# Optimization experiments

Measured on AMD Instinct MI355X. Metric: run time of the kernel, lower is better.

The kernel has to match this reference:

```python
import jax, jax.numpy as jnp
import numpy as np

FP8_MAX = 448.0  # finfo(float8_e4m3fn).max

def setup_inputs() -> dict:
    key = jax.random.key(0)
    k_x, k_w, k_b = jax.random.split(key, 3)
    B, S, D_IN, D_OUT = 4, 2048, 4096, 16384
    x = jax.random.normal(k_x, (B, S, D_IN), dtype=jnp.float32)
    # Build an fp8-quantized weight exactly as FP8WeightOnlyLinear.from_linear does:
    w = jax.random.normal(k_w, (D_OUT, D_IN), dtype=jnp.float32) * 0.02
    amax = jnp.max(jnp.abs(w))
    scale = jnp.where(amax > 0, amax / FP8_MAX, 1.0)
    # round-trip through float8_e4m3fn so stored values are true fp8 codes
    w_fp8 = jnp.clip(w / scale, -FP8_MAX, FP8_MAX).astype(jnp.float8_e4m3fn)
    weight_fp8 = w_fp8.astype(jnp.float32)  # fp8-representable values, held in fp32
    weight_scale = scale.reshape(1).astype(jnp.float32)
    bias = jax.random.normal(k_b, (D_OUT,), dtype=jnp.float32) * 0.01
    return {"x": x, "weight_fp8": weight_fp8, "weight_scale": weight_scale, "bias": bias}

def reference(x, weight_fp8, weight_scale, bias):
    # w = weight_fp8.to(x.dtype) * weight_scale ; out = x @ w.T + bias
    w = weight_fp8.astype(x.dtype) * weight_scale.astype(x.dtype)  # [D_OUT, D_IN]
    out = jnp.einsum('bsd,od->bso', x, w) + bias.astype(x.dtype)
    return out
```

## Files before the change

kernel.cpp:

```cpp
#include <hip/hip_runtime.h>
#include <stdint.h>

typedef unsigned int u32;
using i32x4 = __attribute__((ext_vector_type(4))) int;

#define GLD_LDS16(SRC, DST)                                      \
  __builtin_amdgcn_global_load_lds(                              \
      (const __attribute__((address_space(1))) void*)(SRC),      \
      (__attribute__((address_space(3))) void*)(DST), 16, 0, 0)

#define SCHED0() __builtin_amdgcn_sched_barrier(0)
#define BAR()    __builtin_amdgcn_s_barrier()
#define PRIO(x)  __builtin_amdgcn_s_setprio(x)

__global__ __launch_bounds__(256)
void quant_rows(const float* __restrict__ x, const float* __restrict__ w,
                signed char* __restrict__ xq, signed char* __restrict__ wq,
                float* __restrict__ sx, float* __restrict__ sw,
                int Mrows, int totRows, int K) {
  __shared__ float red[4];
  for (int row = blockIdx.x; row < totRows; row += gridDim.x) {
    const bool isx = row < Mrows;
    const float* src = isx ? x + (size_t)row * K : w + (size_t)(row - Mrows) * K;
    const float4* s4 = reinterpret_cast<const float4*>(src) + threadIdx.x * 4;
    float4 v[4];
#pragma unroll
    for (int g = 0; g < 4; ++g) v[g] = s4[g];
    float am = 0.f;
#pragma unroll
    for (int g = 0; g < 4; ++g)
      am = fmaxf(am, fmaxf(fmaxf(fabsf(v[g].x), fabsf(v[g].y)),
                           fmaxf(fabsf(v[g].z), fabsf(v[g].w))));
#pragma unroll
    for (int m = 1; m <= 32; m <<= 1) am = fmaxf(am, __shfl_xor(am, m));
    if ((threadIdx.x & 63) == 0) red[threadIdx.x >> 6] = am;
    __syncthreads();
    am = fmaxf(fmaxf(red[0], red[1]), fmaxf(red[2], red[3]));
    const float s   = am > 0.f ? am * (1.f / 127.f) : 1.f;
    const float inv = am > 0.f ? 127.f / am : 0.f;
    u32 pk[4];
#pragma unroll
    for (int g = 0; g < 4; ++g) {
      const float* vp = reinterpret_cast<const float*>(&v[g]);
      u32 p = 0;
#pragma unroll
      for (int e = 0; e < 4; ++e) {
        int q = (int)rintf(vp[e] * inv);
        q = q < -127 ? -127 : (q > 127 ? 127 : q);
        p |= ((u32)(q & 0xff)) << (8 * e);
      }
      pk[g] = p;
    }
    signed char* dst = (isx ? xq + (size_t)row * K : wq + (size_t)(row - Mrows) * K)
                       + threadIdx.x * 16;
    *reinterpret_cast<uint4*>(dst) = make_uint4(pk[0], pk[1], pk[2], pk[3]);
    if (threadIdx.x == 0) { if (isx) sx[row] = s; else sw[row - Mrows] = s; }
    __syncthreads();
  }
}

__global__ __launch_bounds__(512, 2)
void gemm_i8(const signed char* __restrict__ A,
             const signed char* __restrict__ B,
             const float* __restrict__ sx,
             const float* __restrict__ sw,
             const float* __restrict__ wscale_p,
             const float* __restrict__ bias,
             float* __restrict__ C,
             int Nn, int Kk, int NT) {
  __shared__ signed char lds[2][2][256 * 64];

  const int tid  = threadIdx.x;
  const int lane = tid & 63;
  const int wave = tid >> 6;
  const int wr = wave >> 2;
  const int wc = wave & 3;

  const int bid = blockIdx.x;
  const int cpx = gridDim.x >> 3;
  const int wg  = (bid & 7) * cpx + (bid >> 3);
  const int mt = wg / NT, nt = wg % NT;
  const int m0 = mt * 256, n0 = nt * 256;

  const int srow = lane >> 2;
  const int ss   = (lane & 3) ^ ((lane >> 3) & 3);
  const int r16  = lane & 15;
  const int kq   = lane >> 4;

  const signed char* ga = A + ((size_t)m0 + wave * 32 + srow) * Kk + ss * 16;
  const signed char* gb = B + ((size_t)n0 + wave * 32 + srow) * Kk + ss * 16;

  const int aoff = (wr * 128 + r16) * 64 + ((kq ^ ((r16 >> 1) & 3)) << 4);
  const int boff = (wc * 64  + r16) * 64 + ((kq ^ ((r16 >> 1) & 3)) << 4);

  i32x4 acc[8][4];
#pragma unroll
  for (int i = 0; i < 8; ++i)
#pragma unroll
    for (int j = 0; j < 4; ++j)
      acc[i][j] = (i32x4){0, 0, 0, 0};

  i32x4 afA[4], afB[4];
  i32x4 bP[4], bQ[4];

#define STAGEI(bfi_, op_, kt_) do {                                             \
    const signed char* _g = ((op_) ? gb : ga) + (size_t)(kt_) * 64;             \
    signed char* _d = &lds[bfi_][op_][wave * 32 * 64];                          \
    GLD_LDS16(_g,                    _d);                                       \
    GLD_LDS16(_g + (size_t)16 * Kk,  _d + 16 * 64);                             \
  } while (0)

#define LDAI(AF_, la_, mh_) do {                                                \
    _Pragma("unroll") for (int _i = 0; _i < 4; ++_i)                            \
      AF_[_i] = *reinterpret_cast<const i32x4*>(                                \
          (la_) + aoff + ((mh_) * 4 + _i) * 1024);                              \
  } while (0)

#define LDBI(BF_, lb_) do {                                                     \
    _Pragma("unroll") for (int _n = 0; _n < 4; ++_n)                            \
      BF_[_n] = *reinterpret_cast<const i32x4*>((lb_) + boff + _n * 1024);      \
  } while (0)

#define MFMAI(mh_, AF_, BF_)                                                    \
  _Pragma("unroll") for (int i = 0; i < 4; ++i)                                 \
  _Pragma("unroll") for (int n = 0; n < 4; ++n)                                 \
    acc[(mh_) * 4 + i][n] = __builtin_amdgcn_mfma_i32_16x16x64_i8(              \
        AF_[i], BF_[n], acc[(mh_) * 4 + i][n], 0, 0, 0)

  const int KT = Kk >> 6;

  STAGEI(0, 0, 0); STAGEI(0, 1, 0);
  STAGEI(1, 0, 1); STAGEI(1, 1, 1);
  asm volatile("s_waitcnt vmcnt(4)" ::: "memory");
  SCHED0(); BAR(); SCHED0();
  LDAI(afA, (const signed char*)&lds[0][0][0], 0);
  LDBI(bP,  (const signed char*)&lds[0][1][0]);

#define TILEI(t_, CUR_, B0_, B1_) do {                                          \
    const signed char* laC = &lds[CUR_][0][0];                                  \
    const signed char* laN = &lds[(CUR_) ^ 1][0][0];                            \
    const signed char* lbN = &lds[(CUR_) ^ 1][1][0];                            \
    const int kt2 = ((t_) + 2 < KT) ? (t_) + 2 : KT - 1;                        \
                                                                        \
    SCHED0(); BAR(); SCHED0();                                                  \
    PRIO(1); MFMAI(0, afA, B0_); PRIO(0);                                       \
    LDAI(afB, laC, 1);                                                          \
    STAGEI(CUR_, 1, kt2);                                                       \
    SCHED0();                                                                   \
    asm volatile("s_waitcnt vmcnt(2)" ::: "memory");                            \
                                                                        \
    SCHED0(); BAR(); SCHED0();                                                  \
    PRIO(1); MFMAI(1, afB, B0_); PRIO(0);                                       \
    LDAI(afA, laN, 0);                                                          \
    LDBI(B1_, lbN);                                                             \
    STAGEI(CUR_, 0, kt2);                                                       \
  } while (0)

  for (int t = 0; t < KT; t += 2) {
    TILEI(t,     0, bP, bQ);
    TILEI(t + 1, 1, bQ, bP);
  }

  const float wsc = wscale_p[0];
  float cw[4], bv[4];
#pragma unroll
  for (int ni = 0; ni < 4; ++ni) {
    const int col = n0 + wc * 64 + ni * 16 + r16;
    cw[ni] = sw[col] * wsc;
    bv[ni] = bias[col];
  }
#pragma unroll
  for (int mi = 0; mi < 8; ++mi) {
#pragma unroll
    for (int r = 0; r < 4; ++r) {
      const int row = m0 + wr * 128 + mi * 16 + kq * 4 + r;
      const float sxr = sx[row];
      float* cp = C + (size_t)row * Nn + (n0 + wc * 64 + r16);
#pragma unroll
      for (int ni = 0; ni < 4; ++ni)
        cp[ni * 16] = (float)acc[mi][ni][r] * (sxr * cw[ni]) + bv[ni];
    }
  }
#undef STAGEI
#undef LDAI
#undef LDBI
#undef MFMAI
#undef TILEI
}

extern "C" void kernel_launch(void* const* d_in, const int* in_sizes, int n_in,
                              void* d_out, int out_size, void* d_ws, size_t ws_size,
                              hipStream_t stream) {
  (void)n_in; (void)out_size; (void)ws_size;
  const float* x  = (const float*)d_in[0];
  const float* w  = (const float*)d_in[1];
  const float* sc = (const float*)d_in[2];
  const float* bs = (const float*)d_in[3];
  float* out = (float*)d_out;

  const int N = in_sizes[3];
  const int K = in_sizes[1] / N;
  const int M = in_sizes[0] / K;

  signed char* xq = (signed char*)d_ws;
  signed char* wq = xq + (size_t)M * K;
  float* sxp = (float*)(wq + (size_t)N * K);
  float* swp = sxp + M;

  quant_rows<<<M + N, 256, 0, stream>>>(x, w, xq, wq, sxp, swp, M, M + N, K);

  const int NT = N / 256;
  const int nwg = (M / 256) * NT;
  gemm_i8<<<nwg, 512, 0, stream>>>(xq, wq, sxp, swp, sc, bs, out, N, K, NT);
}
```

Before: 723.3 us.

## Double GEMM K-tile to 128 with new XOR swizzle and finer MFMA interleave

The int8 GEMM stages 128-wide K slices into LDS instead of 64, which halves the number of barrier-separated main-loop steps. The LDS swizzle is reworked for 128-byte rows, and each half-tile is split into two K sub-steps so that fragment loads interleave with MFMA groups. LDS use grows to 128KB per block, which likely prevents the two blocks per CU requested by the launch bounds and so cuts occupancy.

```diff
diff --git a/kernel.cpp b/kernel.cpp
--- a/kernel.cpp
+++ b/kernel.cpp
@@ -60,15 +60,15 @@
 }
 
 __global__ __launch_bounds__(512, 2)
-void gemm_i8(const signed char* __restrict__ A,
-             const signed char* __restrict__ B,
-             const float* __restrict__ sx,
-             const float* __restrict__ sw,
-             const float* __restrict__ wscale_p,
-             const float* __restrict__ bias,
-             float* __restrict__ C,
-             int Nn, int Kk, int NT) {
-  __shared__ signed char lds[2][2][256 * 64];
+void gemm_i8_bk128(const signed char* __restrict__ A,
+                   const signed char* __restrict__ B,
+                   const float* __restrict__ sx,
+                   const float* __restrict__ sw,
+                   const float* __restrict__ wscale_p,
+                   const float* __restrict__ bias,
+                   float* __restrict__ C,
+                   int Nn, int Kk, int NT) {
+  __shared__ signed char lds[2][2][256 * 128];
 
   const int tid  = threadIdx.x;
   const int lane = tid & 63;
@@ -82,16 +82,16 @@
   const int mt = wg / NT, nt = wg % NT;
   const int m0 = mt * 256, n0 = nt * 256;
 
-  const int srow = lane >> 2;
-  const int ss   = (lane & 3) ^ ((lane >> 3) & 3);
+  const int srow = lane >> 3;
+  const int ss   = (lane & 7) ^ (srow & 7);
   const int r16  = lane & 15;
   const int kq   = lane >> 4;
 
   const signed char* ga = A + ((size_t)m0 + wave * 32 + srow) * Kk + ss * 16;
   const signed char* gb = B + ((size_t)n0 + wave * 32 + srow) * Kk + ss * 16;
 
-  const int aoff = (wr * 128 + r16) * 64 + ((kq ^ ((r16 >> 1) & 3)) << 4);
-  const int boff = (wc * 64  + r16) * 64 + ((kq ^ ((r16 >> 1) & 3)) << 4);
+  const int aoff = (wr * 128 + r16) * 128 + ((kq ^ (r16 & 7)) << 4);
+  const int boff = (wc * 64  + r16) * 128 + ((kq ^ (r16 & 7)) << 4);
 
   i32x4 acc[8][4];
 #pragma unroll
@@ -103,62 +103,71 @@
   i32x4 afA[4], afB[4];
   i32x4 bP[4], bQ[4];
 
-#define STAGEI(bfi_, op_, kt_) do {                                             \
-    const signed char* _g = ((op_) ? gb : ga) + (size_t)(kt_) * 64;             \
-    signed char* _d = &lds[bfi_][op_][wave * 32 * 64];                          \
+#define STAGE128(bfi_, op_, kt_) do {                                           \
+    const signed char* _g = ((op_) ? gb : ga) + (size_t)(kt_) * 128;            \
+    signed char* _d = &lds[bfi_][op_][wave * 32 * 128];                         \
     GLD_LDS16(_g,                    _d);                                       \
-    GLD_LDS16(_g + (size_t)16 * Kk,  _d + 16 * 64);                             \
-  } while (0)
-
-#define LDAI(AF_, la_, mh_) do {                                                \
+    GLD_LDS16(_g + (size_t)8  * Kk,  _d + 1024);                                \
+    GLD_LDS16(_g + (size_t)16 * Kk,  _d + 2048);                                \
+    GLD_LDS16(_g + (size_t)24 * Kk,  _d + 3072);                                \
+  } while (0)
+
+#define LDFA(AF_, la_, mh_, ks_) do {                                           \
     _Pragma("unroll") for (int _i = 0; _i < 4; ++_i)                            \
       AF_[_i] = *reinterpret_cast<const i32x4*>(                                \
-          (la_) + aoff + ((mh_) * 4 + _i) * 1024);                              \
-  } while (0)
-
-#define LDBI(BF_, lb_) do {                                                     \
+          (la_) + ((aoff + ((mh_) * 4 + _i) * 2048) ^ ((ks_) << 6)));           \
+  } while (0)
+
+#define LDFB(BF_, lb_, ks_) do {                                                \
     _Pragma("unroll") for (int _n = 0; _n < 4; ++_n)                            \
-      BF_[_n] = *reinterpret_cast<const i32x4*>((lb_) + boff + _n * 1024);      \
-  } while (0)
-
-#define MFMAI(mh_, AF_, BF_)                                                    \
+      BF_[_n] = *reinterpret_cast<const i32x4*>(                                \
+          (lb_) + ((boff + _n * 2048) ^ ((ks_) << 6)));                         \
+  } while (0)
+
+#define MFMAC(mh_, AF_, BF_)                                                    \
   _Pragma("unroll") for (int i = 0; i < 4; ++i)                                 \
   _Pragma("unroll") for (int n = 0; n < 4; ++n)                                 \
     acc[(mh_) * 4 + i][n] = __builtin_amdgcn_mfma_i32_16x16x64_i8(              \
         AF_[i], BF_[n], acc[(mh_) * 4 + i][n], 0, 0, 0)
 
-  const int KT = Kk >> 6;
-
-  STAGEI(0, 0, 0); STAGEI(0, 1, 0);
-  STAGEI(1, 0, 1); STAGEI(1, 1, 1);
-  asm volatile("s_waitcnt vmcnt(4)" ::: "memory");
+  const int KT = Kk >> 7;
+
+  STAGE128(0, 0, 0); STAGE128(0, 1, 0);
+  STAGE128(1, 0, 1); STAGE128(1, 1, 1);
+  asm volatile("s_waitcnt vmcnt(8)" ::: "memory");
   SCHED0(); BAR(); SCHED0();
-  LDAI(afA, (const signed char*)&lds[0][0][0], 0);
-  LDBI(bP,  (const signed char*)&lds[0][1][0]);
-
-#define TILEI(t_, CUR_, B0_, B1_) do {                                          \
+  LDFA(afA, (const signed char*)&lds[0][0][0], 0, 0);
+  LDFB(bP,  (const signed char*)&lds[0][1][0], 0);
+  LDFB(bQ,  (const signed char*)&lds[0][1][0], 1);
+
+#define TILE128(t_, CUR_) do {                                                  \
     const signed char* laC = &lds[CUR_][0][0];                                  \
     const signed char* laN = &lds[(CUR_) ^ 1][0][0];                            \
     const signed char* lbN = &lds[(CUR_) ^ 1][1][0];                            \
     const int kt2 = ((t_) + 2 < KT) ? (t_) + 2 : KT - 1;                        \
                                                                         \
     SCHED0(); BAR(); SCHED0();                                                  \
-    PRIO(1); MFMAI(0, afA, B0_); PRIO(0);                                       \
-    LDAI(afB, laC, 1);                                                          \
-    STAGEI(CUR_, 1, kt2);                                                       \
+    LDFA(afB, laC, 1, 0);                                                       \
+    PRIO(1); MFMAC(0, afA, bP); PRIO(0);                       \
+    LDFA(afA, laC, 0, 1);                                                       \
+    STAGE128(CUR_, 1, kt2);                                                     \
+    PRIO(1); MFMAC(1, afB, bP); PRIO(0);                       \
+    LDFA(afB, laC, 1, 1);                                                       \
     SCHED0();                                                                   \
-    asm volatile("s_waitcnt vmcnt(2)" ::: "memory");                            \
+    asm volatile("s_waitcnt vmcnt(4)" ::: "memory");                            \
                                                                         \
     SCHED0(); BAR(); SCHED0();                                                  \
-    PRIO(1); MFMAI(1, afB, B0_); PRIO(0);                                       \
-    LDAI(afA, laN, 0);                                                          \
-    LDBI(B1_, lbN);                                                             \
-    STAGEI(CUR_, 0, kt2);                                                       \
+    PRIO(1); MFMAC(0, afA, bQ); PRIO(0);                       \
+    LDFA(afA, laN, 0, 0);                                                       \
+    LDFB(bP, lbN, 0);                                                           \
+    STAGE128(CUR_, 0, kt2);                                                     \
+    PRIO(1); MFMAC(1, afB, bQ); PRIO(0);                       \
+    LDFB(bQ, lbN, 1);                                \
   } while (0)
 
   for (int t = 0; t < KT; t += 2) {
-    TILEI(t,     0, bP, bQ);
-    TILEI(t + 1, 1, bQ, bP);
+    TILE128(t,     0);
+    TILE128(t + 1, 1);
   }
 
   const float wsc = wscale_p[0];
@@ -181,11 +190,11 @@
         cp[ni * 16] = (float)acc[mi][ni][r] * (sxr * cw[ni]) + bv[ni];
     }
   }
-#undef STAGEI
-#undef LDAI
-#undef LDBI
-#undef MFMAI
-#undef TILEI
+#undef STAGE128
+#undef LDFA
+#undef LDFB
+#undef MFMAC
+#undef TILE128
 }
 
 extern "C" void kernel_launch(void* const* d_in, const int* in_sizes, int n_in,
@@ -211,5 +220,5 @@
 
   const int NT = N / 256;
   const int nwg = (M / 256) * NT;
-  gemm_i8<<<nwg, 512, 0, stream>>>(xq, wq, sxp, swp, sc, bs, out, N, K, NT);
+  gemm_i8_bk128<<<nwg, 512, 0, stream>>>(xq, wq, sxp, swp, sc, bs, out, N, K, NT);
 }
```

Result: faster. 629.0 us (median of 2 runs) (-13.0%).
